# Kernel optimization log

Hardware: AMD Instinct MI355X
Metric: run time of the kernel (lower is better)

Reference implementation:

```python
import jax, jax.numpy as jnp
import numpy as np

N_NODES = 100000
N_EDGES = 1000000
DIM = 64
N_GRAPHS = 256
OUT_DIM = 10
BN_EPS = 1e-5


def setup_inputs() -> dict:
    key = jax.random.key(0)
    ks = jax.random.split(key, 12)
    s = 0.1  # weight init scale
    x = jax.random.normal(ks[0], (N_NODES, DIM), jnp.float32)
    edge_index = jax.random.randint(ks[1], (2, N_EDGES), 0, N_NODES, dtype=jnp.int32)
    batch = jnp.sort(jax.random.randint(ks[2], (N_NODES,), 0, N_GRAPHS, dtype=jnp.int32))
    w1 = jax.random.normal(ks[3], (3, DIM, DIM), jnp.float32) * s
    b1 = jax.random.normal(ks[4], (3, DIM), jnp.float32) * s
    w2 = jax.random.normal(ks[5], (3, DIM, DIM), jnp.float32) * s
    b2 = jax.random.normal(ks[6], (3, DIM), jnp.float32) * s
    gamma = jax.random.uniform(ks[7], (3, DIM), jnp.float32, 0.5, 1.5)
    beta = jax.random.normal(ks[8], (3, DIM), jnp.float32) * s
    eps_g = jnp.zeros((3,), jnp.float32)  # GIN train_eps, init 0
    lin_w = jax.random.normal(ks[9], (DIM, OUT_DIM), jnp.float32) * s
    lin_b = jax.random.normal(ks[10], (OUT_DIM,), jnp.float32) * s
    return dict(x=x, edge_index=edge_index, batch=batch, w1=w1, b1=b1,
                w2=w2, b2=b2, gamma=gamma, beta=beta, eps_g=eps_g,
                lin_w=lin_w, lin_b=lin_b)


def _gin_layer(x, src, dst, w1, b1, w2, b2, gamma, beta, eps):
    # scatter-add neighbor aggregation: agg[i] = sum_{(j->i) in E} x[j]
    agg = jax.ops.segment_sum(x[src], dst, num_segments=N_NODES)
    h = (1.0 + eps) * x + agg
    h = jax.nn.relu(h @ w1 + b1)
    h = jax.nn.relu(h @ w2 + b2)
    # BatchNorm1d, training-mode batch statistics (biased variance)
    mean = jnp.mean(h, axis=0)
    var = jnp.mean((h - mean) ** 2, axis=0)
    h = (h - mean) * jax.lax.rsqrt(var + BN_EPS) * gamma + beta
    return jax.nn.relu(h)  # outer F.relu(conv(...))


def reference(x, edge_index, batch, w1, b1, w2, b2, gamma, beta, eps_g, lin_w, lin_b):
    src, dst = edge_index[0], edge_index[1]
    for i in range(3):
        x = _gin_layer(x, src, dst, w1[i], b1[i], w2[i], b2[i],
                       gamma[i], beta[i], eps_g[i])
    # global mean pool over graphs
    sums = jax.ops.segment_sum(x, batch, num_segments=N_GRAPHS)
    counts = jax.ops.segment_sum(jnp.ones((x.shape[0],), x.dtype), batch,
                                 num_segments=N_GRAPHS)
    pooled = sums / jnp.maximum(counts, 1.0)[:, None]
    return pooled @ lin_w + lin_b
```

## Files before the change

kernel.cpp:

```cpp
#include <hip/hip_runtime.h>
#include <hip/hip_bf16.h>

#define N_NODES 100000
#define N_EDGES 1000000
#define DIM 64
#define N_GRAPHS 256
#define OUT_DIM 10
#define BN_EPS 1e-5f

#define POOL_BLOCKS 512
#define LAYER_BLOCKS ((N_NODES + 63) / 64)
#define PAD 24
#define SPILL_CAP 8192
#define NPART 8
#define PART_SZ ((N_NODES + NPART - 1) / NPART)

typedef __bf16 bf16x8 __attribute__((ext_vector_type(8)));
typedef float f32x4 __attribute__((ext_vector_type(4)));

__global__ __launch_bounds__(256) void fill_kernel(
    const int* __restrict__ ei, int* __restrict__ deg,
    int* __restrict__ esrc, int* __restrict__ nspill, int* __restrict__ spill)
{
    const int part = blockIdx.x & (NPART - 1);
    const int e = (blockIdx.x >> 3) * 256 + threadIdx.x;
    if (e >= N_EDGES) return;
    int dst = ei[N_EDGES + e];
    int lo = part * PART_SZ;
    if (dst < lo || dst >= lo + PART_SZ) return;
    int src = ei[e];
    int pos = atomicAdd(&deg[dst], 1);
    if (pos < PAD) {
        esrc[dst * PAD + pos] = src;
    } else {
        int sp = atomicAdd(nspill, 1);
        if (sp < SPILL_CAP) { spill[2 * sp] = dst; spill[2 * sp + 1] = src; }
    }
}

__global__ __launch_bounds__(64) void bnprep_kernel(
    const float* __restrict__ sums, const float* __restrict__ gamma,
    const float* __restrict__ beta, float* __restrict__ sc)
{
    int d = threadIdx.x;
    const float inv_n = 1.0f / (float)N_NODES;
    float mean = sums[d] * inv_n;
    float m2 = sums[64 + d] * inv_n;
    float var = m2 - mean * mean;
    float scale = gamma[d] * rsqrtf(var + BN_EPS);
    sc[d] = scale;
    sc[64 + d] = fmaf(-mean, scale, beta[d]);
}

__global__ __launch_bounds__(256) void wprep_kernel(
    const float* __restrict__ w1, const float* __restrict__ w2,
    __bf16* __restrict__ wf)
{
    int L = blockIdx.x >> 1, mat = blockIdx.x & 1;
    const float* w = (mat ? w2 : w1) + L * 4096;
    __bf16* dst = wf + blockIdx.x * 8192;
#pragma unroll
    for (int r = 0; r < 2; ++r) {
        int idx = threadIdx.x + 256 * r;
        int lane = idx & 63;
        int kt = idx >> 6;
        int kstep = kt >> 2, nt = kt & 3;
        int n = nt * 16 + (lane & 15);
        int kbase = kstep * 32 + (lane >> 4) * 8;
#pragma unroll
        for (int j = 0; j < 8; ++j) {
            float v = w[(kbase + j) * 64 + n];
            __bf16 hi = (__bf16)v;
            dst[idx * 8 + j] = hi;
            dst[4096 + idx * 8 + j] = (__bf16)(v - (float)hi);
        }
    }
}

template <bool BN>
__global__ __launch_bounds__(256) void layer_kernel(
    const float* __restrict__ x, const float* __restrict__ sc,
    const int* __restrict__ deg, const int* __restrict__ esrc,
    const int* __restrict__ nspill, const int* __restrict__ spill,
    float* __restrict__ h2out,
    const __bf16* __restrict__ wf1, const __bf16* __restrict__ wf2,
    const float* __restrict__ b1, const float* __restrict__ b2,
    const float* __restrict__ eps_all, int layer,
    float* __restrict__ sums)
{
    __shared__ __attribute__((aligned(16))) unsigned tile[4][16][68];
    __shared__ float bnacc[128];

    const int tid = threadIdx.x;
    const int lane = tid & 63;
    const int wv = tid >> 6;
    const int q = lane >> 4;
    const int r = lane & 15;
    const int node0 = blockIdx.x * 64 + wv * 16;
    const bool active = node0 < N_NODES;

    if (tid < 128) bnacc[tid] = 0.0f;

    f32x4 acc[4];
    float bs[4], bq[4];
#pragma unroll
    for (int nt = 0; nt < 4; ++nt) {
        acc[nt] = (f32x4){0.f, 0.f, 0.f, 0.f};
        bs[nt] = 0.0f; bq[nt] = 0.0f;
    }

    float scale = 1.0f, shift = 0.0f;
    if (BN) { scale = sc[lane]; shift = sc[64 + lane]; }

    if (active) {
        const float epsv = 1.0f + eps_all[layer];

        int dvec = 0;
        if (lane < 16) dvec = deg[node0 + lane];
        uint4 nf0, nf1, nf2;
        {
            const uint4* ip = (const uint4*)(esrc + (size_t)node0 * PAD);
            nf0 = ip[0]; nf1 = ip[1]; nf2 = ip[2];
        }
        for (int i = 0; i < 16; ++i) {
            const uint4 c0 = nf0, c1 = nf1, c2 = nf2;
            if (i < 15) {
                const uint4* ip = (const uint4*)(esrc + (size_t)(node0 + i + 1) * PAD);
                nf0 = ip[0]; nf1 = ip[1]; nf2 = ip[2];
            }
            const int n = node0 + i;
            const int dfull = __builtin_amdgcn_readlane(dvec, i);
            const int d = min(dfull, PAD);

            float xv = x[(size_t)n * 64 + lane];
            if (BN) xv = fmaxf(fmaf(xv, scale, shift), 0.0f);
            float hval = epsv * xv;

            {
                unsigned idx[12] = {c0.x, c0.y, c0.z, c0.w, c1.x, c1.y,
                                    c1.z, c1.w, c2.x, c2.y, c2.z, c2.w};
                float v[12];
#pragma unroll
                for (int j = 0; j < 12; ++j) {
                    unsigned s = idx[j];
                    s = (s < (unsigned)N_NODES) ? s : 0u;
                    v[j] = x[(size_t)s * 64 + lane];
                }
#pragma unroll
                for (int j = 0; j < 12; ++j) {
                    float t = v[j];
                    if (BN) t = fmaxf(fmaf(t, scale, shift), 0.0f);
                    hval += (j < d) ? t : 0.0f;
                }
            }
            if (d > 12) {
                const int* ep = esrc + (size_t)n * PAD + 12;
                float v[12];
#pragma unroll
                for (int j = 0; j < 12; ++j) {
                    unsigned s = (unsigned)ep[j];
                    s = (s < (unsigned)N_NODES) ? s : 0u;
                    v[j] = x[(size_t)s * 64 + lane];
                }
#pragma unroll
                for (int j = 0; j < 12; ++j) {
                    float t = v[j];
                    if (BN) t = fmaxf(fmaf(t, scale, shift), 0.0f);
                    hval += (12 + j < d) ? t : 0.0f;
                }
            }
            if (dfull > PAD) {
                int ns = min(*nspill, SPILL_CAP);
                for (int e = 0; e < ns; ++e) {
                    if (spill[2 * e] == n) {
                        float t = x[(size_t)spill[2 * e + 1] * 64 + lane];
                        if (BN) t = fmaxf(fmaf(t, scale, shift), 0.0f);
                        hval += t;
                    }
                }
            }
            __bf16 hi = (__bf16)hval;
            __bf16 lo = (__bf16)(hval - (float)hi);
            tile[wv][i][lane] = ((unsigned)__builtin_bit_cast(unsigned short, hi) << 16)
                              | (unsigned)__builtin_bit_cast(unsigned short, lo);
        }

        uint4 f0 = *(const uint4*)&tile[wv][r][q * 8];
        uint4 f1 = *(const uint4*)&tile[wv][r][q * 8 + 4];
        uint4 f2 = *(const uint4*)&tile[wv][r][32 + q * 8];
        uint4 f3 = *(const uint4*)&tile[wv][r][32 + q * 8 + 4];
#pragma unroll
        for (int kstep = 0; kstep < 2; ++kstep) {
            uint4 p0 = kstep ? f2 : f0;
            uint4 p1 = kstep ? f3 : f1;
            unsigned pk[8] = {p0.x, p0.y, p0.z, p0.w, p1.x, p1.y, p1.z, p1.w};
            bf16x8 ahi, alo;
#pragma unroll
            for (int j = 0; j < 8; ++j) {
                ahi[j] = __builtin_bit_cast(__bf16, (unsigned short)(pk[j] >> 16));
                alo[j] = __builtin_bit_cast(__bf16, (unsigned short)(pk[j] & 0xffffu));
            }
#pragma unroll
            for (int nt = 0; nt < 4; ++nt) {
                const __bf16* bp = wf1 + ((kstep * 4 + nt) * 64 + lane) * 8;
                bf16x8 bhi = *(const bf16x8*)bp;
                bf16x8 blo = *(const bf16x8*)(bp + 4096);
                acc[nt] = __builtin_amdgcn_mfma_f32_16x16x32_bf16(ahi, bhi, acc[nt], 0, 0, 0);
                acc[nt] = __builtin_amdgcn_mfma_f32_16x16x32_bf16(alo, bhi, acc[nt], 0, 0, 0);
                acc[nt] = __builtin_amdgcn_mfma_f32_16x16x32_bf16(ahi, blo, acc[nt], 0, 0, 0);
            }
        }
#pragma unroll
        for (int nt = 0; nt < 4; ++nt) {
            float b1v = b1[nt * 16 + r];
#pragma unroll
            for (int reg = 0; reg < 4; ++reg) {
                float v = fmaxf(acc[nt][reg] + b1v, 0.0f);
                __bf16 hi = (__bf16)v;
                __bf16 lo = (__bf16)(v - (float)hi);
                unsigned pk = ((unsigned)__builtin_bit_cast(unsigned short, hi) << 16)
                            | (unsigned)__builtin_bit_cast(unsigned short, lo);
                tile[wv][q * 4 + reg][nt * 16 + r] = pk;
            }
            acc[nt] = (f32x4){0.f, 0.f, 0.f, 0.f};
        }
#pragma unroll
        for (int kstep = 0; kstep < 2; ++kstep) {
            uint4 p0 = *(const uint4*)&tile[wv][r][kstep * 32 + q * 8];
            uint4 p1 = *(const uint4*)&tile[wv][r][kstep * 32 + q * 8 + 4];
            unsigned pk[8] = {p0.x, p0.y, p0.z, p0.w, p1.x, p1.y, p1.z, p1.w};
            bf16x8 ahi, alo;
#pragma unroll
            for (int j = 0; j < 8; ++j) {
                ahi[j] = __builtin_bit_cast(__bf16, (unsigned short)(pk[j] >> 16));
                alo[j] = __builtin_bit_cast(__bf16, (unsigned short)(pk[j] & 0xffffu));
            }
#pragma unroll
            for (int nt = 0; nt < 4; ++nt) {
                const __bf16* bp = wf2 + ((kstep * 4 + nt) * 64 + lane) * 8;
                bf16x8 bhi = *(const bf16x8*)bp;
                bf16x8 blo = *(const bf16x8*)(bp + 4096);
                acc[nt] = __builtin_amdgcn_mfma_f32_16x16x32_bf16(ahi, bhi, acc[nt], 0, 0, 0);
                acc[nt] = __builtin_amdgcn_mfma_f32_16x16x32_bf16(alo, bhi, acc[nt], 0, 0, 0);
                acc[nt] = __builtin_amdgcn_mfma_f32_16x16x32_bf16(ahi, blo, acc[nt], 0, 0, 0);
            }
        }
#pragma unroll
        for (int nt = 0; nt < 4; ++nt) {
            float b2v = b2[nt * 16 + r];
#pragma unroll
            for (int reg = 0; reg < 4; ++reg) {
                float v = fmaxf(acc[nt][reg] + b2v, 0.0f);
                h2out[(size_t)(node0 + q * 4 + reg) * 64 + nt * 16 + r] = v;
                bs[nt] += v;
                bq[nt] = fmaf(v, v, bq[nt]);
            }
        }
    }
    __syncthreads();
#pragma unroll
    for (int nt = 0; nt < 4; ++nt) {
        float s = bs[nt];
        s += __shfl_xor(s, 16);
        s += __shfl_xor(s, 32);
        float ss = bq[nt];
        ss += __shfl_xor(ss, 16);
        ss += __shfl_xor(ss, 32);
        if (q == 0) {
            atomicAdd(&bnacc[nt * 16 + r], s);
            atomicAdd(&bnacc[64 + nt * 16 + r], ss);
        }
    }
    __syncthreads();
    if (tid < 128) unsafeAtomicAdd(&sums[tid], bnacc[tid]);
}

__global__ __launch_bounds__(256) void pool_kernel(
    const float* __restrict__ h2, const float* __restrict__ sc,
    const int* __restrict__ batch,
    float* __restrict__ pooled, float* __restrict__ counts)
{
    const int lane = threadIdx.x & 63;
    const int w = blockIdx.x * 4 + (threadIdx.x >> 6);
    const int nw = POOL_BLOCKS * 4;
    const int npw = (N_NODES + nw - 1) / nw;
    int n0 = w * npw;
    if (n0 >= N_NODES) return;
    int n1 = n0 + npw;
    if (n1 > N_NODES) n1 = N_NODES;

    const float scale = sc[lane];
    const float shift = sc[64 + lane];

    int cur = batch[n0];
    float acc = 0.0f, cnt = 0.0f;
    for (int n = n0; n < n1; ++n) {
        int g = batch[n];
        if (g != cur) {
            unsafeAtomicAdd(&pooled[cur * 64 + lane], acc);
            if (lane == 0) unsafeAtomicAdd(&counts[cur], cnt);
            acc = 0.0f; cnt = 0.0f; cur = g;
        }
        float v = h2[(size_t)n * 64 + lane];
        v = fmaxf(fmaf(v, scale, shift), 0.0f);
        acc += v;
        cnt += 1.0f;
    }
    unsafeAtomicAdd(&pooled[cur * 64 + lane], acc);
    if (lane == 0) unsafeAtomicAdd(&counts[cur], cnt);
}

__global__ __launch_bounds__(256) void final_kernel(
    const float* __restrict__ pooled, const float* __restrict__ counts,
    const float* __restrict__ lin_w, const float* __restrict__ lin_b,
    float* __restrict__ out)
{
    int t = blockIdx.x * 256 + threadIdx.x;
    if (t >= N_GRAPHS * OUT_DIM) return;
    int g = t / OUT_DIM;
    int o = t - g * OUT_DIM;
    float acc = 0.0f;
#pragma unroll 8
    for (int d = 0; d < 64; ++d)
        acc = fmaf(pooled[g * 64 + d], lin_w[d * OUT_DIM + o], acc);
    float c = fmaxf(counts[g], 1.0f);
    out[t] = acc / c + lin_b[o];
}

extern "C" void kernel_launch(void* const* d_in, const int* in_sizes, int n_in,
                              void* d_out, int out_size, void* d_ws, size_t ws_size,
                              hipStream_t stream)
{
    const float* x0    = (const float*)d_in[0];
    const int*   ei    = (const int*)d_in[1];
    const int*   batch = (const int*)d_in[2];
    const float* w1    = (const float*)d_in[3];
    const float* b1    = (const float*)d_in[4];
    const float* w2    = (const float*)d_in[5];
    const float* b2    = (const float*)d_in[6];
    const float* gamma = (const float*)d_in[7];
    const float* beta  = (const float*)d_in[8];
    const float* eps_g = (const float*)d_in[9];
    const float* lin_w = (const float*)d_in[10];
    const float* lin_b = (const float*)d_in[11];
    float* out = (float*)d_out;

    float* ws   = (float*)d_ws;
    float* A    = ws;
    float* B    = ws + (size_t)N_NODES * 64;
    float* SUMS = ws + (size_t)2 * N_NODES * 64;
    float* POOL = SUMS + 384;
    float* CNT  = POOL + N_GRAPHS * 64;
    int*   DEG    = (int*)(CNT + N_GRAPHS);
    int*   NSPILL = DEG + N_NODES;
    float* SC   = (float*)(NSPILL + 16);
    __bf16* WF  = (__bf16*)(SC + 384);
    int*   SPILL  = (int*)(WF + 6 * 8192);
    int*   ESRC   = SPILL + 2 * SPILL_CAP;

    const size_t zero_bytes = (384 + N_GRAPHS * 64 + N_GRAPHS) * sizeof(float)
                            + (N_NODES + 16) * sizeof(int);
    const int fill_blocks = ((N_EDGES + 255) / 256) * NPART;

    hipMemsetAsync(SUMS, 0, zero_bytes, stream);
    wprep_kernel<<<6, 256, 0, stream>>>(w1, w2, WF);
    fill_kernel<<<fill_blocks, 256, 0, stream>>>(ei, DEG, ESRC, NSPILL, SPILL);

    layer_kernel<false><<<LAYER_BLOCKS, 256, 0, stream>>>(
        x0, nullptr, DEG, ESRC, NSPILL, SPILL, A,
        WF, WF + 8192, b1, b2, eps_g, 0, SUMS);
    bnprep_kernel<<<1, 64, 0, stream>>>(SUMS, gamma, beta, SC);

    layer_kernel<true><<<LAYER_BLOCKS, 256, 0, stream>>>(
        A, SC, DEG, ESRC, NSPILL, SPILL, B,
        WF + 16384, WF + 24576, b1 + 64, b2 + 64, eps_g, 1, SUMS + 128);
    bnprep_kernel<<<1, 64, 0, stream>>>(SUMS + 128, gamma + 64, beta + 64, SC + 128);

    layer_kernel<true><<<LAYER_BLOCKS, 256, 0, stream>>>(
        B, SC + 128, DEG, ESRC, NSPILL, SPILL, A,
        WF + 32768, WF + 40960, b1 + 128, b2 + 128, eps_g, 2, SUMS + 256);
    bnprep_kernel<<<1, 64, 0, stream>>>(SUMS + 256, gamma + 128, beta + 128, SC + 256);

    pool_kernel<<<POOL_BLOCKS, 256, 0, stream>>>(A, SC + 256, batch, POOL, CNT);
    final_kernel<<<(N_GRAPHS * OUT_DIM + 255) / 256, 256, 0, stream>>>(
        POOL, CNT, lin_w, lin_b, out);
}
```

Measured before the change: 396.2 us.

## Gather neighbor features from a bf16 shadow copy instead of fp32

Adds a bf16 copy of the node features, made by a cast kernel for the input and written alongside the fp32 output by each layer. Neighbor gathers in the aggregation now read 2-byte values, which halves the bytes pulled by the random-access scatter-sum. The self term still reads fp32. The cost is an extra bf16 write per layer, an extra cast pass, and lower precision in the aggregated sums, which may affect accuracy tolerance.

```diff
diff --git a/kernel.cpp b/kernel.cpp
--- a/kernel.cpp
+++ b/kernel.cpp
@@ -38,6 +38,20 @@
     }
 }
 
+__global__ __launch_bounds__(256) void xcast_kernel(
+    const float4* __restrict__ xin, ushort4* __restrict__ xout)
+{
+    int t = blockIdx.x * 256 + threadIdx.x;
+    if (t >= N_NODES * 16) return;
+    float4 v = xin[t];
+    ushort4 o;
+    o.x = __builtin_bit_cast(unsigned short, (__bf16)v.x);
+    o.y = __builtin_bit_cast(unsigned short, (__bf16)v.y);
+    o.z = __builtin_bit_cast(unsigned short, (__bf16)v.z);
+    o.w = __builtin_bit_cast(unsigned short, (__bf16)v.w);
+    xout[t] = o;
+}
+
 __global__ __launch_bounds__(64) void bnprep_kernel(
     const float* __restrict__ sums, const float* __restrict__ gamma,
     const float* __restrict__ beta, float* __restrict__ sc)
@@ -79,10 +93,11 @@
 
 template <bool BN>
 __global__ __launch_bounds__(256) void layer_kernel(
-    const float* __restrict__ x, const float* __restrict__ sc,
+    const float* __restrict__ x, const unsigned short* __restrict__ xb,
+    const float* __restrict__ sc,
     const int* __restrict__ deg, const int* __restrict__ esrc,
     const int* __restrict__ nspill, const int* __restrict__ spill,
-    float* __restrict__ h2out,
+    float* __restrict__ h2out, unsigned short* __restrict__ xbout,
     const __bf16* __restrict__ wf1, const __bf16* __restrict__ wf2,
     const float* __restrict__ b1, const float* __restrict__ b2,
     const float* __restrict__ eps_all, int layer,
@@ -139,32 +154,32 @@
             {
                 unsigned idx[12] = {c0.x, c0.y, c0.z, c0.w, c1.x, c1.y,
                                     c1.z, c1.w, c2.x, c2.y, c2.z, c2.w};
-                float v[12];
+                unsigned short u[12];
 #pragma unroll
                 for (int j = 0; j < 12; ++j) {
                     unsigned s = idx[j];
                     s = (s < (unsigned)N_NODES) ? s : 0u;
-                    v[j] = x[(size_t)s * 64 + lane];
+                    u[j] = xb[(size_t)s * 64 + lane];
                 }
 #pragma unroll
                 for (int j = 0; j < 12; ++j) {
-                    float t = v[j];
+                    float t = (float)__builtin_bit_cast(__bf16, u[j]);
                     if (BN) t = fmaxf(fmaf(t, scale, shift), 0.0f);
                     hval += (j < d) ? t : 0.0f;
                 }
             }
             if (d > 12) {
                 const int* ep = esrc + (size_t)n * PAD + 12;
-                float v[12];
+                unsigned short u[12];
 #pragma unroll
                 for (int j = 0; j < 12; ++j) {
                     unsigned s = (unsigned)ep[j];
                     s = (s < (unsigned)N_NODES) ? s : 0u;
-                    v[j] = x[(size_t)s * 64 + lane];
+                    u[j] = xb[(size_t)s * 64 + lane];
                 }
 #pragma unroll
                 for (int j = 0; j < 12; ++j) {
-                    float t = v[j];
+                    float t = (float)__builtin_bit_cast(__bf16, u[j]);
                     if (BN) t = fmaxf(fmaf(t, scale, shift), 0.0f);
                     hval += (12 + j < d) ? t : 0.0f;
                 }
@@ -173,7 +188,8 @@
                 int ns = min(*nspill, SPILL_CAP);
                 for (int e = 0; e < ns; ++e) {
                     if (spill[2 * e] == n) {
-                        float t = x[(size_t)spill[2 * e + 1] * 64 + lane];
+                        float t = (float)__builtin_bit_cast(
+                            __bf16, xb[(size_t)spill[2 * e + 1] * 64 + lane]);
                         if (BN) t = fmaxf(fmaf(t, scale, shift), 0.0f);
                         hval += t;
                     }
@@ -251,7 +267,9 @@
 #pragma unroll
             for (int reg = 0; reg < 4; ++reg) {
                 float v = fmaxf(acc[nt][reg] + b2v, 0.0f);
-                h2out[(size_t)(node0 + q * 4 + reg) * 64 + nt * 16 + r] = v;
+                size_t oi = (size_t)(node0 + q * 4 + reg) * 64 + nt * 16 + r;
+                h2out[oi] = v;
+                xbout[oi] = __builtin_bit_cast(unsigned short, (__bf16)v);
                 bs[nt] += v;
                 bq[nt] = fmaf(v, v, bq[nt]);
             }
@@ -357,27 +375,32 @@
     __bf16* WF  = (__bf16*)(SC + 384);
     int*   SPILL  = (int*)(WF + 6 * 8192);
     int*   ESRC   = SPILL + 2 * SPILL_CAP;
+    unsigned short* XP = (unsigned short*)(ESRC + (size_t)N_NODES * PAD);
+    unsigned short* XQ = XP + (size_t)N_NODES * 64;
+    unsigned short* XR = XQ + (size_t)N_NODES * 64;
 
     const size_t zero_bytes = (384 + N_GRAPHS * 64 + N_GRAPHS) * sizeof(float)
                             + (N_NODES + 16) * sizeof(int);
     const int fill_blocks = ((N_EDGES + 255) / 256) * NPART;
+    const int elem_blocks = (N_NODES * 16 + 255) / 256;
 
     hipMemsetAsync(SUMS, 0, zero_bytes, stream);
     wprep_kernel<<<6, 256, 0, stream>>>(w1, w2, WF);
+    xcast_kernel<<<elem_blocks, 256, 0, stream>>>((const float4*)x0, (ushort4*)XP);
     fill_kernel<<<fill_blocks, 256, 0, stream>>>(ei, DEG, ESRC, NSPILL, SPILL);
 
     layer_kernel<false><<<LAYER_BLOCKS, 256, 0, stream>>>(
-        x0, nullptr, DEG, ESRC, NSPILL, SPILL, A,
+        x0, XP, nullptr, DEG, ESRC, NSPILL, SPILL, A, XQ,
         WF, WF + 8192, b1, b2, eps_g, 0, SUMS);
     bnprep_kernel<<<1, 64, 0, stream>>>(SUMS, gamma, beta, SC);
 
     layer_kernel<true><<<LAYER_BLOCKS, 256, 0, stream>>>(
-        A, SC, DEG, ESRC, NSPILL, SPILL, B,
+        A, XQ, SC, DEG, ESRC, NSPILL, SPILL, B, XP,
         WF + 16384, WF + 24576, b1 + 64, b2 + 64, eps_g, 1, SUMS + 128);
     bnprep_kernel<<<1, 64, 0, stream>>>(SUMS + 128, gamma + 64, beta + 64, SC + 128);
 
     layer_kernel<true><<<LAYER_BLOCKS, 256, 0, stream>>>(
-        B, SC + 128, DEG, ESRC, NSPILL, SPILL, A,
+        B, XP, SC + 128, DEG, ESRC, NSPILL, SPILL, A, XR,
         WF + 32768, WF + 40960, b1 + 128, b2 + 128, eps_g, 2, SUMS + 256);
     bnprep_kernel<<<1, 64, 0, stream>>>(SUMS + 256, gamma + 128, beta + 128, SC + 256);
 
```

Measured after the change: 398.2 us. Within noise of the previous version (+0.5%).
